# Optimization experiments

Measured on AMD Instinct MI355X. Metric: run time of the kernel, lower is better.

The kernel has to match this reference:

```python
import jax, jax.numpy as jnp
import numpy as np

D_MODEL = 2048
NUM_HEADS = 16
NUM_KV_HEADS = 4
HEAD_DIM = D_MODEL // NUM_HEADS  # 128
THETA = 10000.0


def _rotate_half(x):
    # interleaved rotate: pairs (x0,x1) -> (-x1, x0)
    x1 = x[..., ::2]
    x2 = x[..., 1::2]
    return jnp.stack((-x2, x1), axis=-1).reshape(x.shape)


def _rope_cos_sin(seq_len, dtype):
    inv_freq = 1.0 / (THETA ** (jnp.arange(0, HEAD_DIM, 2, dtype=jnp.float32) / HEAD_DIM))
    pos = jnp.arange(seq_len, dtype=jnp.float32)
    freqs = pos[:, None] * inv_freq[None, :]            # [S, HD/2]
    emb = jnp.repeat(freqs, 2, axis=-1)                  # [S, HD] interleaved
    return jnp.cos(emb).astype(dtype), jnp.sin(emb).astype(dtype)


def setup_inputs() -> dict:
    key = jax.random.key(0)
    ks = jax.random.split(key, 5)
    B, S = 2, 2048
    x = jax.random.normal(ks[0], (B, S, D_MODEL), dtype=jnp.float32)
    scale = 0.02
    wq = jax.random.normal(ks[1], (D_MODEL, NUM_HEADS * HEAD_DIM), dtype=jnp.float32) * scale
    wk = jax.random.normal(ks[2], (D_MODEL, NUM_KV_HEADS * HEAD_DIM), dtype=jnp.float32) * scale
    wv = jax.random.normal(ks[3], (D_MODEL, NUM_KV_HEADS * HEAD_DIM), dtype=jnp.float32) * scale
    wo = jax.random.normal(ks[4], (D_MODEL, D_MODEL), dtype=jnp.float32) * scale
    return {"x": x, "wq": wq, "wk": wk, "wv": wv, "wo": wo}


def reference(x, wq, wk, wv, wo):
    B, S, _ = x.shape
    q = (x @ wq).reshape(B, S, NUM_HEADS, HEAD_DIM).transpose(0, 2, 1, 3)      # [B,H,S,D]
    k = (x @ wk).reshape(B, S, NUM_KV_HEADS, HEAD_DIM).transpose(0, 2, 1, 3)   # [B,KV,S,D]
    v = (x @ wv).reshape(B, S, NUM_KV_HEADS, HEAD_DIM).transpose(0, 2, 1, 3)

    cos, sin = _rope_cos_sin(S, q.dtype)
    cos = cos[None, None]  # [1,1,S,HD]
    sin = sin[None, None]
    q = q * cos + _rotate_half(q) * sin
    k = k * cos + _rotate_half(k) * sin

    reps = NUM_HEADS // NUM_KV_HEADS
    k = jnp.repeat(k, reps, axis=1)  # [B,H,S,D]
    v = jnp.repeat(v, reps, axis=1)

    scale = 1.0 / jnp.sqrt(jnp.asarray(HEAD_DIM, dtype=q.dtype))
    scores = jnp.einsum('bhqd,bhkd->bhqk', q, k) * scale
    causal = jnp.tril(jnp.ones((S, S), dtype=bool))
    scores = jnp.where(causal[None, None], scores, jnp.finfo(scores.dtype).min)
    attn = jax.nn.softmax(scores, axis=-1)
    y = jnp.einsum('bhqk,bhkd->bhqd', attn, v)            # [B,H,S,D]
    y = y.transpose(0, 2, 1, 3).reshape(B, S, NUM_HEADS * HEAD_DIM)
    return y @ wo
```

## Files before the change

kernel.cpp:

```cpp
#include <hip/hip_runtime.h>
#include <hip/hip_bf16.h>
#include <stdint.h>

typedef __hip_bfloat16 bf16;
typedef __attribute__((ext_vector_type(8))) short short8;
typedef __attribute__((ext_vector_type(4))) float f32x4;

#define D_MODEL 2048
#define NHEADS 16
#define NKV 4
#define HD 128
#define BATCH 2
#define SEQ 2048
#define NTOK (BATCH*SEQ)
#define QKV_N 3072
#define QSCALE 0.08838834764831845f
#define QSCALE_L2E (0.08838834764831845f * 1.4426950408889634f)

__global__ __launch_bounds__(256) void trig_kernel(float2* __restrict__ tab) {
    int idx = blockIdx.x * 256 + threadIdx.x;
    int s = idx >> 6, i = idx & 63;
    double inv_freq = pow(10000.0, -(double)i / 64.0);
    double sn, cs;
    sincos((double)s * inv_freq, &sn, &cs);
    tab[idx] = make_float2((float)cs, (float)sn);
}

__global__ __launch_bounds__(256) void conv8(const float* __restrict__ in,
                                             bf16* __restrict__ out, int n8) {
    int idx = blockIdx.x * 256 + threadIdx.x;
    if (idx >= n8) return;
    const float4* p = (const float4*)(in + (size_t)idx * 8);
    float4 a = p[0], b = p[1];
    union { short8 v; bf16 e[8]; } u;
    u.e[0] = __float2bfloat16(a.x); u.e[1] = __float2bfloat16(a.y);
    u.e[2] = __float2bfloat16(a.z); u.e[3] = __float2bfloat16(a.w);
    u.e[4] = __float2bfloat16(b.x); u.e[5] = __float2bfloat16(b.y);
    u.e[6] = __float2bfloat16(b.z); u.e[7] = __float2bfloat16(b.w);
    *(short8*)(out + (size_t)idx * 8) = u.v;
}

#define TILE_LD 68
__global__ __launch_bounds__(256) void ct64(const float* __restrict__ in,
                                            bf16* __restrict__ out, int K, int N) {
    __shared__ float tile[64 * TILE_LD];
    int n0 = blockIdx.x * 64, k0 = blockIdx.y * 64;
    int t = threadIdx.x;
#pragma unroll
    for (int i = 0; i < 4; ++i) {
        int idx = t + 256 * i;
        int r = idx >> 4;
        int c4 = (idx & 15) * 4;
        *(float4*)&tile[r * TILE_LD + c4] = *(const float4*)(in + (size_t)(k0 + r) * N + n0 + c4);
    }
    __syncthreads();
#pragma unroll
    for (int i = 0; i < 2; ++i) {
        int idx = t + 256 * i;
        int n = idx >> 3;
        int kc = (idx & 7) * 8;
        union { short8 v; bf16 e[8]; } u;
#pragma unroll
        for (int j = 0; j < 8; ++j) u.e[j] = __float2bfloat16(tile[(kc + j) * TILE_LD + n]);
        *(short8*)(out + (size_t)(n0 + n) * K + k0 + kc) = u.v;
    }
}

__global__ __launch_bounds__(256) void vt64(const bf16* __restrict__ qkvb,
                                            bf16* __restrict__ vT) {
    __shared__ bf16 tile[64 * 72];
    int vd0 = blockIdx.x * 64, s0 = blockIdx.y * 64, b = blockIdx.z;
    int t = threadIdx.x;
#pragma unroll
    for (int i = 0; i < 2; ++i) {
        int idx = t + 256 * i;
        int r = idx >> 3;
        int c8 = (idx & 7) * 8;
        *(int4*)&tile[r * 72 + c8] =
            *(const int4*)(qkvb + (size_t)(b * SEQ + s0 + r) * QKV_N + 2560 + vd0 + c8);
    }
    __syncthreads();
#pragma unroll
    for (int i = 0; i < 2; ++i) {
        int idx = t + 256 * i;
        int vd = idx >> 3;
        int s8 = (idx & 7) * 8;
        union { short8 v; bf16 e[8]; } u;
#pragma unroll
        for (int j = 0; j < 8; ++j) u.e[j] = tile[(s8 + j) * 72 + vd];
        *(short8*)(vT + (size_t)(b * 512 + vd0 + vd) * 2048 + s0 + s8) = u.v;
    }
}

template <typename OutT, bool ROPE>
__global__ __launch_bounds__(256) void gemm_bt32(const bf16* __restrict__ A,
                                                 const bf16* __restrict__ Bt,
                                                 OutT* __restrict__ C, int M, int N, int K,
                                                 const float2* __restrict__ trig) {
    __shared__ bf16 As[128 * 32];
    __shared__ bf16 Bs[128 * 32];
    const int GX = gridDim.x;
    const int nwg = GX * gridDim.y;
    const int lin = blockIdx.y * GX + blockIdx.x;
    const int swz = (lin & 7) * (nwg >> 3) + (lin >> 3);
    const int m0 = (swz / GX) * 128, n0 = (swz % GX) * 128;
    const int tid = threadIdx.x;
    const int wave = tid >> 6, lane = tid & 63;
    const int wr = wave >> 1, wc = wave & 1;
    const int l15 = lane & 15, g = lane >> 4;
    const int srow = lane >> 2;
    const int sk8 = 8 * ((lane & 3) ^ ((srow >> 1) & 3));
    const int rsw = ((l15 >> 1) & 3) << 3;
    f32x4 acc[4][4] = {};

    for (int k0 = 0; k0 < K; k0 += 32) {
        __syncthreads();
#pragma unroll
        for (int i = 0; i < 2; ++i) {
            int chunk = wave * 2 + i;
            const bf16* ga = A + (size_t)(m0 + chunk * 16 + srow) * K + k0 + sk8;
            bf16* la = As + chunk * 512 + lane * 8;
            __builtin_amdgcn_global_load_lds((const __attribute__((address_space(1))) void*)ga,
                                             (__attribute__((address_space(3))) void*)la, 16, 0, 0);
            const bf16* gb = Bt + (size_t)(n0 + chunk * 16 + srow) * K + k0 + sk8;
            bf16* lb = Bs + chunk * 512 + lane * 8;
            __builtin_amdgcn_global_load_lds((const __attribute__((address_space(1))) void*)gb,
                                             (__attribute__((address_space(3))) void*)lb, 16, 0, 0);
        }
        __syncthreads();
        short8 af[4], bfr[4];
#pragma unroll
        for (int mi = 0; mi < 4; ++mi)
            af[mi] = *(const short8*)&As[(wr * 64 + mi * 16 + l15) * 32 + ((g * 8) ^ rsw)];
#pragma unroll
        for (int ni = 0; ni < 4; ++ni)
            bfr[ni] = *(const short8*)&Bs[(wc * 64 + ni * 16 + l15) * 32 + ((g * 8) ^ rsw)];
#pragma unroll
        for (int mi = 0; mi < 4; ++mi)
#pragma unroll
            for (int ni = 0; ni < 4; ++ni)
                acc[mi][ni] = __builtin_amdgcn_mfma_f32_16x16x32_bf16(af[mi], bfr[ni], acc[mi][ni], 0, 0, 0);
    }
#pragma unroll
    for (int mi = 0; mi < 4; ++mi)
#pragma unroll
        for (int ni = 0; ni < 4; ++ni) {
            int row = m0 + wr * 64 + mi * 16 + g * 4;
            int col = n0 + wc * 64 + ni * 16 + l15;
#pragma unroll
            for (int r = 0; r < 4; ++r) {
                float v = acc[mi][ni][r];
                if constexpr (ROPE) {
                    float partner = __shfl_xor(v, 1);
                    if (col < 2560) {
                        int s = (row + r) & (SEQ - 1);
                        int i2 = (col & 127) >> 1;
                        float2 t = trig[s * 64 + i2];
                        v = (col & 1) ? (v * t.x + partner * t.y)
                                      : (v * t.x - partner * t.y);
                    }
                    if (col < 2048) v *= QSCALE_L2E;
                }
                if constexpr (__is_same(OutT, float))
                    C[(size_t)(row + r) * N + col] = v;
                else
                    C[(size_t)(row + r) * N + col] = __float2bfloat16(v);
            }
        }
}

template <typename OutT>
__global__ __launch_bounds__(256) void gemm_bt64(const bf16* __restrict__ A,
                                                 const bf16* __restrict__ Bt,
                                                 OutT* __restrict__ C, int M, int N, int K) {
    __shared__ bf16 As[128 * 64];
    __shared__ bf16 Bs[128 * 64];
    const int GX = gridDim.x;
    const int nwg = GX * gridDim.y;
    const int lin = blockIdx.y * GX + blockIdx.x;
    const int swz = (lin & 7) * (nwg >> 3) + (lin >> 3);
    const int m0 = (swz / GX) * 128, n0 = (swz % GX) * 128;
    const int tid = threadIdx.x;
    const int wave = tid >> 6, lane = tid & 63;
    const int wr = wave >> 1, wc = wave & 1;
    const int l15 = lane & 15, g = lane >> 4;
    f32x4 acc[4][4] = {};

    const bf16* ga[4];
    const bf16* gb[4];
#pragma unroll
    for (int i = 0; i < 4; ++i) {
        int cidx = tid + 256 * i;
        int r = cidx >> 3, j = cidx & 7;
        int sc = 8 * (j ^ (r & 7));
        ga[i] = A + (size_t)(m0 + r) * K + sc;
        gb[i] = Bt + (size_t)(n0 + r) * K + sc;
    }

    for (int k0 = 0; k0 < K; k0 += 64) {
        __syncthreads();
#pragma unroll
        for (int i = 0; i < 4; ++i) {
            int cidx = tid + 256 * i;
            __builtin_amdgcn_global_load_lds(
                (const __attribute__((address_space(1))) void*)ga[i],
                (__attribute__((address_space(3))) void*)(As + cidx * 8), 16, 0, 0);
            __builtin_amdgcn_global_load_lds(
                (const __attribute__((address_space(1))) void*)gb[i],
                (__attribute__((address_space(3))) void*)(Bs + cidx * 8), 16, 0, 0);
            ga[i] += 64;
            gb[i] += 64;
        }
        __syncthreads();
#pragma unroll
        for (int kk = 0; kk < 2; ++kk) {
            short8 af[4], bfr[4];
#pragma unroll
            for (int mi = 0; mi < 4; ++mi) {
                int row = wr * 64 + mi * 16 + l15;
                af[mi] = *(const short8*)&As[row * 64 + ((kk * 32 + g * 8) ^ ((row & 7) << 3))];
            }
#pragma unroll
            for (int ni = 0; ni < 4; ++ni) {
                int row = wc * 64 + ni * 16 + l15;
                bfr[ni] = *(const short8*)&Bs[row * 64 + ((kk * 32 + g * 8) ^ ((row & 7) << 3))];
            }
#pragma unroll
            for (int mi = 0; mi < 4; ++mi)
#pragma unroll
                for (int ni = 0; ni < 4; ++ni)
                    acc[mi][ni] = __builtin_amdgcn_mfma_f32_16x16x32_bf16(af[mi], bfr[ni], acc[mi][ni], 0, 0, 0);
        }
    }
#pragma unroll
    for (int mi = 0; mi < 4; ++mi)
#pragma unroll
        for (int ni = 0; ni < 4; ++ni) {
            int row = m0 + wr * 64 + mi * 16 + g * 4;
            int col = n0 + wc * 64 + ni * 16 + l15;
#pragma unroll
            for (int r = 0; r < 4; ++r) {
                float v = acc[mi][ni][r];
                if constexpr (__is_same(OutT, float))
                    C[(size_t)(row + r) * N + col] = v;
                else
                    C[(size_t)(row + r) * N + col] = __float2bfloat16(v);
            }
        }
}

#define PL_LD 72
__global__ __launch_bounds__(256) void attn10(const bf16* __restrict__ qkv,
                                              const bf16* __restrict__ vT,
                                              bf16* __restrict__ y) {
    const int bx = blockIdx.x, h = blockIdx.y, b = blockIdx.z;
    const int kvh = h >> 2;
    const int tid = threadIdx.x, wave = tid >> 6, lane = tid & 63;
    const int l15 = lane & 15, g = lane >> 4;
    __shared__ bf16 Ks[64 * 128];
    __shared__ bf16 Vt[128 * 64];
    __shared__ bf16 Pl[4][16 * PL_LD];
    bf16* plw = Pl[0] + wave * 16 * PL_LD;

    for (int half = 0; half < 2; ++half) {
        const int qt = half ? (31 - bx) : bx;
        const int qrow0 = qt * 64 + wave * 16;
        short8 qf[4];
        {
            const bf16* qp = qkv + (size_t)(b * SEQ + qrow0 + l15) * QKV_N + h * HD + g * 8;
#pragma unroll
            for (int c = 0; c < 4; ++c) qf[c] = *(const short8*)(qp + c * 32);
        }
        f32x4 acc[8] = {};
        float m_[4], lsum[4];
#pragma unroll
        for (int r = 0; r < 4; ++r) { m_[r] = -3.0e38f; lsum[r] = 0.f; }

        const bf16* gk[4];
        const bf16* gv[4];
#pragma unroll
        for (int i = 0; i < 4; ++i) {
            int cidx = tid + 256 * i;
            int key = cidx >> 4, j = cidx & 15;
            gk[i] = qkv + (size_t)(b * SEQ + key) * QKV_N + D_MODEL + kvh * HD + 8 * (j ^ (key & 7));
            int d = cidx >> 3, j2 = cidx & 7;
            gv[i] = vT + (size_t)(b * 512 + kvh * HD + d) * 2048 + 8 * (j2 ^ (d & 7));
        }

        const int diag_kv0 = qt * 64;
        for (int kv0 = 0; kv0 <= diag_kv0; kv0 += 64) {
#pragma unroll
            for (int i = 0; i < 4; ++i) {
                int cidx = tid + 256 * i;
                __builtin_amdgcn_global_load_lds(
                    (const __attribute__((address_space(1))) void*)gk[i],
                    (__attribute__((address_space(3))) void*)(Ks + cidx * 8), 16, 0, 0);
                __builtin_amdgcn_global_load_lds(
                    (const __attribute__((address_space(1))) void*)gv[i],
                    (__attribute__((address_space(3))) void*)(Vt + cidx * 8), 16, 0, 0);
                gk[i] += 64 * QKV_N;
                gv[i] += 64;
            }
            __syncthreads();

            f32x4 sc[4];
            __builtin_amdgcn_s_setprio(1);
#pragma unroll
            for (int ct = 0; ct < 4; ++ct) {
                sc[ct] = (f32x4){0.f, 0.f, 0.f, 0.f};
                int key = ct * 16 + l15;
                int ksw = (key & 7) << 3;
#pragma unroll
                for (int c = 0; c < 4; ++c) {
                    short8 kf = *(const short8*)&Ks[key * 128 + ((c * 32 + g * 8) ^ ksw)];
                    sc[ct] = __builtin_amdgcn_mfma_f32_16x16x32_bf16(qf[c], kf, sc[ct], 0, 0, 0);
                }
            }
            __builtin_amdgcn_s_setprio(0);
            if (kv0 == diag_kv0) {
                int qbase = qrow0 + g * 4;
#pragma unroll
                for (int ct = 0; ct < 4; ++ct) {
                    int key = kv0 + ct * 16 + l15;
#pragma unroll
                    for (int r = 0; r < 4; ++r)
                        if (key > qbase + r) sc[ct][r] = -3.0e38f;
                }
            }
#pragma unroll
            for (int r = 0; r < 4; ++r) {
                float pmax = fmaxf(fmaxf(sc[0][r], sc[1][r]), fmaxf(sc[2][r], sc[3][r]));
                if (__any(pmax > m_[r] + 8.0f)) {
                    float mx = pmax;
#pragma unroll
                    for (int o = 1; o < 16; o <<= 1) mx = fmaxf(mx, __shfl_xor(mx, o));
                    float mn = fmaxf(m_[r], mx);
                    float alpha = exp2f(m_[r] - mn);
                    m_[r] = mn;
                    lsum[r] *= alpha;
#pragma unroll
                    for (int nt = 0; nt < 8; ++nt) acc[nt][r] *= alpha;
                }
                float p0 = exp2f(sc[0][r] - m_[r]);
                float p1 = exp2f(sc[1][r] - m_[r]);
                float p2 = exp2f(sc[2][r] - m_[r]);
                float p3 = exp2f(sc[3][r] - m_[r]);
                int row = g * 4 + r;
                plw[row * PL_LD + l15]      = __float2bfloat16(p0);
                plw[row * PL_LD + 16 + l15] = __float2bfloat16(p1);
                plw[row * PL_LD + 32 + l15] = __float2bfloat16(p2);
                plw[row * PL_LD + 48 + l15] = __float2bfloat16(p3);
                lsum[r] += (p0 + p1) + (p2 + p3);
            }
            short8 pf0 = *(const short8*)&plw[l15 * PL_LD + g * 8];
            short8 pf1 = *(const short8*)&plw[l15 * PL_LD + 32 + g * 8];
            __builtin_amdgcn_s_setprio(1);
#pragma unroll
            for (int nt = 0; nt < 8; ++nt) {
                int d = nt * 16 + l15;
                int dsw = (d & 7) << 3;
                short8 vf0 = *(const short8*)&Vt[d * 64 + ((g * 8) ^ dsw)];
                short8 vf1 = *(const short8*)&Vt[d * 64 + ((32 + g * 8) ^ dsw)];
                acc[nt] = __builtin_amdgcn_mfma_f32_16x16x32_bf16(pf0, vf0, acc[nt], 0, 0, 0);
                acc[nt] = __builtin_amdgcn_mfma_f32_16x16x32_bf16(pf1, vf1, acc[nt], 0, 0, 0);
            }
            __builtin_amdgcn_s_setprio(0);
            __syncthreads();
        }
        float linv[4];
#pragma unroll
        for (int r = 0; r < 4; ++r) {
            float ls = lsum[r];
#pragma unroll
            for (int o = 1; o < 16; o <<= 1) ls += __shfl_xor(ls, o);
            linv[r] = 1.0f / ls;
        }
        int qrow = qrow0 + g * 4;
#pragma unroll
        for (int nt = 0; nt < 8; ++nt) {
            int d = nt * 16 + l15;
#pragma unroll
            for (int r = 0; r < 4; ++r)
                y[(size_t)(b * SEQ + qrow + r) * D_MODEL + h * HD + d] =
                    __float2bfloat16(acc[nt][r] * linv[r]);
        }
        __syncthreads();
    }
}

extern "C" void kernel_launch(void* const* d_in, const int* in_sizes, int n_in,
                              void* d_out, int out_size, void* d_ws, size_t ws_size,
                              hipStream_t stream) {
    const float* x  = (const float*)d_in[0];
    const float* wq = (const float*)d_in[1];
    const float* wk = (const float*)d_in[2];
    const float* wv = (const float*)d_in[3];
    const float* wo = (const float*)d_in[4];

    bf16*   qkvb  = (bf16*)d_ws;
    bf16*   ybb   = (bf16*)d_ws + (size_t)NTOK * 3072;
    bf16*   woT   = (bf16*)d_ws + (size_t)NTOK * 3072 + (size_t)NTOK * D_MODEL;
    bf16*   xb    = (bf16*)d_out;
    bf16*   wqkvT = (bf16*)d_out + (size_t)NTOK * D_MODEL;
    float2* trig  = (float2*)((bf16*)d_out + (size_t)NTOK * D_MODEL + (size_t)QKV_N * D_MODEL);
    bf16*   vT    = (bf16*)d_out;
    float*  outf  = (float*)d_out;

    conv8<<<dim3(NTOK * D_MODEL / (256 * 8)), 256, 0, stream>>>(x, xb, NTOK * D_MODEL / 8);
    ct64<<<dim3(32, 32), 256, 0, stream>>>(wq, wqkvT, 2048, 2048);
    ct64<<<dim3(8, 32), 256, 0, stream>>>(wk, wqkvT + (size_t)2048 * 2048, 2048, 512);
    ct64<<<dim3(8, 32), 256, 0, stream>>>(wv, wqkvT + (size_t)2560 * 2048, 2048, 512);
    ct64<<<dim3(32, 32), 256, 0, stream>>>(wo, woT, 2048, 2048);
    trig_kernel<<<dim3(SEQ * 64 / 256), 256, 0, stream>>>(trig);

    gemm_bt32<bf16, true><<<dim3(QKV_N / 128, NTOK / 128), 256, 0, stream>>>(
        xb, wqkvT, qkvb, NTOK, QKV_N, D_MODEL, trig);

    vt64<<<dim3(8, 32, BATCH), 256, 0, stream>>>(qkvb, vT);

    attn10<<<dim3(16, NHEADS, BATCH), 256, 0, stream>>>(qkvb, vT, ybb);

    gemm_bt64<float><<<dim3(D_MODEL / 128, NTOK / 128), 256, 0, stream>>>(
        ybb, woT, outf, NTOK, D_MODEL, D_MODEL);
}
```

Before: 239.3 us.

## Split V projection into separate GEMM writing transposed V directly

The fused QKV GEMM is split into a Q/K GEMM with RoPE and a separate V GEMM whose epilogue writes V already transposed. This removes the standalone V-transpose kernel and its round trip through the qkv buffer. In exchange there is an extra GEMM launch with a small grid (4x32 tiles) that may underuse the GPU. The V GEMM's epilogue also does strided 8-byte stores.

```diff
diff --git a/kernel.cpp b/kernel.cpp
--- a/kernel.cpp
+++ b/kernel.cpp
@@ -13,7 +13,7 @@
 #define BATCH 2
 #define SEQ 2048
 #define NTOK (BATCH*SEQ)
-#define QKV_N 3072
+#define QKN 2560
 #define QSCALE 0.08838834764831845f
 #define QSCALE_L2E (0.08838834764831845f * 1.4426950408889634f)
 
@@ -66,37 +66,10 @@
     }
 }
 
-__global__ __launch_bounds__(256) void vt64(const bf16* __restrict__ qkvb,
-                                            bf16* __restrict__ vT) {
-    __shared__ bf16 tile[64 * 72];
-    int vd0 = blockIdx.x * 64, s0 = blockIdx.y * 64, b = blockIdx.z;
-    int t = threadIdx.x;
-#pragma unroll
-    for (int i = 0; i < 2; ++i) {
-        int idx = t + 256 * i;
-        int r = idx >> 3;
-        int c8 = (idx & 7) * 8;
-        *(int4*)&tile[r * 72 + c8] =
-            *(const int4*)(qkvb + (size_t)(b * SEQ + s0 + r) * QKV_N + 2560 + vd0 + c8);
-    }
-    __syncthreads();
-#pragma unroll
-    for (int i = 0; i < 2; ++i) {
-        int idx = t + 256 * i;
-        int vd = idx >> 3;
-        int s8 = (idx & 7) * 8;
-        union { short8 v; bf16 e[8]; } u;
-#pragma unroll
-        for (int j = 0; j < 8; ++j) u.e[j] = tile[(s8 + j) * 72 + vd];
-        *(short8*)(vT + (size_t)(b * 512 + vd0 + vd) * 2048 + s0 + s8) = u.v;
-    }
-}
-
-template <typename OutT, bool ROPE>
-__global__ __launch_bounds__(256) void gemm_bt32(const bf16* __restrict__ A,
-                                                 const bf16* __restrict__ Bt,
-                                                 OutT* __restrict__ C, int M, int N, int K,
-                                                 const float2* __restrict__ trig) {
+__global__ __launch_bounds__(256) void gemm_qk(const bf16* __restrict__ A,
+                                               const bf16* __restrict__ Bt,
+                                               bf16* __restrict__ C, int M, int N, int K,
+                                               const float2* __restrict__ trig) {
     __shared__ bf16 As[128 * 32];
     __shared__ bf16 Bs[128 * 32];
     const int GX = gridDim.x;
@@ -150,22 +123,76 @@
 #pragma unroll
             for (int r = 0; r < 4; ++r) {
                 float v = acc[mi][ni][r];
-                if constexpr (ROPE) {
-                    float partner = __shfl_xor(v, 1);
-                    if (col < 2560) {
-                        int s = (row + r) & (SEQ - 1);
-                        int i2 = (col & 127) >> 1;
-                        float2 t = trig[s * 64 + i2];
-                        v = (col & 1) ? (v * t.x + partner * t.y)
-                                      : (v * t.x - partner * t.y);
-                    }
-                    if (col < 2048) v *= QSCALE_L2E;
-                }
-                if constexpr (__is_same(OutT, float))
-                    C[(size_t)(row + r) * N + col] = v;
-                else
-                    C[(size_t)(row + r) * N + col] = __float2bfloat16(v);
-            }
+                float partner = __shfl_xor(v, 1);
+                int s = (row + r) & (SEQ - 1);
+                int i2 = (col & 127) >> 1;
+                float2 t = trig[s * 64 + i2];
+                v = (col & 1) ? (v * t.x + partner * t.y)
+                              : (v * t.x - partner * t.y);
+                if (col < 2048) v *= QSCALE_L2E;
+                C[(size_t)(row + r) * N + col] = __float2bfloat16(v);
+            }
+        }
+}
+
+__global__ __launch_bounds__(256) void gemm_vt(const bf16* __restrict__ A,
+                                               const bf16* __restrict__ Bt,
+                                               bf16* __restrict__ vT, int M, int N, int K) {
+    __shared__ bf16 As[128 * 32];
+    __shared__ bf16 Bs[128 * 32];
+    const int GX = gridDim.x;
+    const int nwg = GX * gridDim.y;
+    const int lin = blockIdx.y * GX + blockIdx.x;
+    const int swz = (lin & 7) * (nwg >> 3) + (lin >> 3);
+    const int m0 = (swz / GX) * 128, n0 = (swz % GX) * 128;
+    const int tid = threadIdx.x;
+    const int wave = tid >> 6, lane = tid & 63;
+    const int wr = wave >> 1, wc = wave & 1;
+    const int l15 = lane & 15, g = lane >> 4;
+    const int srow = lane >> 2;
+    const int sk8 = 8 * ((lane & 3) ^ ((srow >> 1) & 3));
+    const int rsw = ((l15 >> 1) & 3) << 3;
+    f32x4 acc[4][4] = {};
+
+    for (int k0 = 0; k0 < K; k0 += 32) {
+        __syncthreads();
+#pragma unroll
+        for (int i = 0; i < 2; ++i) {
+            int chunk = wave * 2 + i;
+            const bf16* ga = A + (size_t)(m0 + chunk * 16 + srow) * K + k0 + sk8;
+            bf16* la = As + chunk * 512 + lane * 8;
+            __builtin_amdgcn_global_load_lds((const __attribute__((address_space(1))) void*)ga,
+                                             (__attribute__((address_space(3))) void*)la, 16, 0, 0);
+            const bf16* gb = Bt + (size_t)(n0 + chunk * 16 + srow) * K + k0 + sk8;
+            bf16* lb = Bs + chunk * 512 + lane * 8;
+            __builtin_amdgcn_global_load_lds((const __attribute__((address_space(1))) void*)gb,
+                                             (__attribute__((address_space(3))) void*)lb, 16, 0, 0);
+        }
+        __syncthreads();
+        short8 af[4], bfr[4];
+#pragma unroll
+        for (int mi = 0; mi < 4; ++mi)
+            af[mi] = *(const short8*)&As[(wr * 64 + mi * 16 + l15) * 32 + ((g * 8) ^ rsw)];
+#pragma unroll
+        for (int ni = 0; ni < 4; ++ni)
+            bfr[ni] = *(const short8*)&Bs[(wc * 64 + ni * 16 + l15) * 32 + ((g * 8) ^ rsw)];
+#pragma unroll
+        for (int mi = 0; mi < 4; ++mi)
+#pragma unroll
+            for (int ni = 0; ni < 4; ++ni)
+                acc[mi][ni] = __builtin_amdgcn_mfma_f32_16x16x32_bf16(af[mi], bfr[ni], acc[mi][ni], 0, 0, 0);
+    }
+#pragma unroll
+    for (int mi = 0; mi < 4; ++mi)
+#pragma unroll
+        for (int ni = 0; ni < 4; ++ni) {
+            int row = m0 + wr * 64 + mi * 16 + g * 4;
+            int col = n0 + wc * 64 + ni * 16 + l15;
+            int bb = row >> 11, ss = row & 2047;
+            union { ushort4 u4; bf16 e[4]; } pk;
+#pragma unroll
+            for (int r = 0; r < 4; ++r) pk.e[r] = __float2bfloat16(acc[mi][ni][r]);
+            *(ushort4*)(vT + (size_t)(bb * 512 + col) * 2048 + ss) = pk.u4;
         }
 }
 
@@ -267,7 +294,7 @@
         const int qrow0 = qt * 64 + wave * 16;
         short8 qf[4];
         {
-            const bf16* qp = qkv + (size_t)(b * SEQ + qrow0 + l15) * QKV_N + h * HD + g * 8;
+            const bf16* qp = qkv + (size_t)(b * SEQ + qrow0 + l15) * QKN + h * HD + g * 8;
 #pragma unroll
             for (int c = 0; c < 4; ++c) qf[c] = *(const short8*)(qp + c * 32);
         }
@@ -282,7 +309,7 @@
         for (int i = 0; i < 4; ++i) {
             int cidx = tid + 256 * i;
             int key = cidx >> 4, j = cidx & 15;
-            gk[i] = qkv + (size_t)(b * SEQ + key) * QKV_N + D_MODEL + kvh * HD + 8 * (j ^ (key & 7));
+            gk[i] = qkv + (size_t)(b * SEQ + key) * QKN + 2048 + kvh * HD + 8 * (j ^ (key & 7));
             int d = cidx >> 3, j2 = cidx & 7;
             gv[i] = vT + (size_t)(b * 512 + kvh * HD + d) * 2048 + 8 * (j2 ^ (d & 7));
         }
@@ -298,7 +325,7 @@
                 __builtin_amdgcn_global_load_lds(
                     (const __attribute__((address_space(1))) void*)gv[i],
                     (__attribute__((address_space(3))) void*)(Vt + cidx * 8), 16, 0, 0);
-                gk[i] += 64 * QKV_N;
+                gk[i] += 64 * QKN;
                 gv[i] += 64;
             }
             __syncthreads();
@@ -397,26 +424,27 @@
     const float* wv = (const float*)d_in[3];
     const float* wo = (const float*)d_in[4];
 
-    bf16*   qkvb  = (bf16*)d_ws;
-    bf16*   ybb   = (bf16*)d_ws + (size_t)NTOK * 3072;
-    bf16*   woT   = (bf16*)d_ws + (size_t)NTOK * 3072 + (size_t)NTOK * D_MODEL;
-    bf16*   xb    = (bf16*)d_out;
-    bf16*   wqkvT = (bf16*)d_out + (size_t)NTOK * D_MODEL;
-    float2* trig  = (float2*)((bf16*)d_out + (size_t)NTOK * D_MODEL + (size_t)QKV_N * D_MODEL);
-    bf16*   vT    = (bf16*)d_out;
-    float*  outf  = (float*)d_out;
+    bf16*   qkvb = (bf16*)d_ws;
+    bf16*   ybb  = (bf16*)d_ws + (size_t)NTOK * QKN;
+    bf16*   woT  = (bf16*)d_ws + (size_t)NTOK * QKN + (size_t)NTOK * D_MODEL;
+    bf16*   vT   = woT + (size_t)D_MODEL * D_MODEL;
+    bf16*   xb   = (bf16*)d_out;
+    bf16*   wqkT = (bf16*)d_out + (size_t)NTOK * D_MODEL;
+    bf16*   wvT  = wqkT + (size_t)QKN * D_MODEL;
+    float2* trig = (float2*)(wvT + (size_t)512 * D_MODEL);
+    float*  outf = (float*)d_out;
 
     conv8<<<dim3(NTOK * D_MODEL / (256 * 8)), 256, 0, stream>>>(x, xb, NTOK * D_MODEL / 8);
-    ct64<<<dim3(32, 32), 256, 0, stream>>>(wq, wqkvT, 2048, 2048);
-    ct64<<<dim3(8, 32), 256, 0, stream>>>(wk, wqkvT + (size_t)2048 * 2048, 2048, 512);
-    ct64<<<dim3(8, 32), 256, 0, stream>>>(wv, wqkvT + (size_t)2560 * 2048, 2048, 512);
+    ct64<<<dim3(32, 32), 256, 0, stream>>>(wq, wqkT, 2048, 2048);
+    ct64<<<dim3(8, 32), 256, 0, stream>>>(wk, wqkT + (size_t)2048 * 2048, 2048, 512);
+    ct64<<<dim3(8, 32), 256, 0, stream>>>(wv, wvT, 2048, 512);
     ct64<<<dim3(32, 32), 256, 0, stream>>>(wo, woT, 2048, 2048);
     trig_kernel<<<dim3(SEQ * 64 / 256), 256, 0, stream>>>(trig);
 
-    gemm_bt32<bf16, true><<<dim3(QKV_N / 128, NTOK / 128), 256, 0, stream>>>(
-        xb, wqkvT, qkvb, NTOK, QKV_N, D_MODEL, trig);
-
-    vt64<<<dim3(8, 32, BATCH), 256, 0, stream>>>(qkvb, vT);
+    gemm_qk<<<dim3(QKN / 128, NTOK / 128), 256, 0, stream>>>(
+        xb, wqkT, qkvb, NTOK, QKN, D_MODEL, trig);
+    gemm_vt<<<dim3(512 / 128, NTOK / 128), 256, 0, stream>>>(
+        xb, wvT, vT, NTOK, 512, D_MODEL);
 
     attn10<<<dim3(16, NHEADS, BATCH), 256, 0, stream>>>(qkvb, vT, ybb);
 
```

New measurement: 289.1 us. 20.8% more time.
